# Kernel optimization log

Hardware: AMD Instinct MI355X
Metric: run time of the kernel (lower is better)

Reference implementation:

```python
import jax, jax.numpy as jnp
import numpy as np


def setup_inputs() -> dict:
    key = jax.random.key(0)
    k1, k2 = jax.random.split(key)
    B, S, K, N = 2, 4096, 4096, 4096
    x = jax.random.randint(k1, (B, S, K), -127, 128, dtype=jnp.int32).astype(jnp.int8)
    weight = jax.random.randint(k2, (N, K), -127, 128, dtype=jnp.int32).astype(jnp.int8)
    bias = jnp.zeros((1, N), dtype=jnp.int8)
    a = jnp.float32(0.01)   # alpha = input_scale * weight_scale / output_scale
    b = jnp.float32(1.0)    # beta = bias_scale / output_scale
    return {"x": x, "weight": weight, "bias": bias, "a": a, "b": b}


def reference(x, weight, bias, a, b):
    # i8gemm.linear_a8_w8_b8_o8: int8 GEMM with int32 accumulation, then
    # y_int8 = saturate_cast(round(alpha * acc + beta * bias)).
    x_shape = x.shape
    xf = x.reshape(-1, x_shape[-1])                     # [M, K] int8
    acc = jnp.matmul(xf, weight.T, preferred_element_type=jnp.int32)  # [M, N]
    y = a * acc.astype(jnp.float32) + b * bias.astype(jnp.float32)    # fused epilogue
    yq = jnp.clip(jnp.round(y), -128.0, 127.0).astype(jnp.int8)       # requantize o8
    return yq.reshape(*x_shape[:-1], -1)
```

## Files before the change

### kernel.cpp

```cpp
#include <hip/hip_runtime.h>
#include <stdint.h>

#define M_DIM 8192
#define N_DIM 4096
#define K_DIM 4096

using int4v = __attribute__((ext_vector_type(4))) int;

__global__ __launch_bounds__(256) void pack_kernel(const int4* __restrict__ sx,
                                                   const int4* __restrict__ sw,
                                                   unsigned int* __restrict__ dst,
                                                   int nx, int ntot) {
    int idx = blockIdx.x * blockDim.x + threadIdx.x;
    if (idx >= ntot) return;
    int4 v = (idx < nx) ? sx[idx] : sw[idx - nx];
    dst[idx] = (v.x & 0xff) | ((v.y & 0xff) << 8) | ((v.z & 0xff) << 16) |
               ((v.w & 0xff) << 24);
}

__device__ __forceinline__ void async_copy16(const char* g, char* l) {
    __builtin_amdgcn_global_load_lds(
        (const __attribute__((address_space(1))) char*)g,
        (__attribute__((address_space(3))) char*)l, 16, 0, 0);
}

__global__ __launch_bounds__(256, 2) void gemm_i8_kernel(
    const char* __restrict__ Aq,
    const char* __restrict__ Bq,
    const int* __restrict__ bias,
    const float* __restrict__ a_ptr,
    const float* __restrict__ b_ptr,
    int32_t* __restrict__ out)
{
    __shared__ char As[128 * 64];
    __shared__ char Bs[256 * 64];

    const int tid  = threadIdx.x;
    const int lane = tid & 63;
    const int wave = tid >> 6;
    const int wr   = wave >> 1;
    const int wc   = wave & 1;
    const int m0   = blockIdx.y * 128;
    const int n0   = blockIdx.x * 256;

    const float alpha = *a_ptr;
    const float beta  = *b_ptr;

    int4v acc[4][8] = {};

    const int srow = tid >> 2;
    const int scol = ((tid & 3) ^ ((srow >> 1) & 3)) * 16;

    const char* aG0 = Aq + (size_t)(m0 + srow) * K_DIM + scol;
    const char* aG1 = aG0 + (size_t)64 * K_DIM;
    const char* bG0 = Bq + (size_t)(n0 + srow) * K_DIM + scol;
    const char* bG1 = bG0 + (size_t)64 * K_DIM;
    const char* bG2 = bG0 + (size_t)128 * K_DIM;
    const char* bG3 = bG0 + (size_t)192 * K_DIM;
    char* aL0 = &As[tid * 16];
    char* aL1 = &As[tid * 16 + 4096];
    char* bL0 = &Bs[tid * 16];
    char* bL1 = &Bs[tid * 16 + 4096];
    char* bL2 = &Bs[tid * 16 + 8192];
    char* bL3 = &Bs[tid * 16 + 12288];

    const int fr  = lane & 15;
    const int gw  = lane >> 4;
    const int fko = (gw ^ ((fr >> 1) & 3)) * 16;

    for (int k0 = 0; k0 < K_DIM; k0 += 64) {
        async_copy16(aG0 + k0, aL0);
        async_copy16(aG1 + k0, aL1);
        async_copy16(bG0 + k0, bL0);
        async_copy16(bG1 + k0, bL1);
        async_copy16(bG2 + k0, bL2);
        async_copy16(bG3 + k0, bL3);
        __syncthreads();

        int4v af[4], bf[8];
#pragma unroll
        for (int i = 0; i < 4; ++i)
            af[i] = *(const int4v*)&As[(wr * 64 + i * 16 + fr) * 64 + fko];
#pragma unroll
        for (int j = 0; j < 8; ++j)
            bf[j] = *(const int4v*)&Bs[(wc * 128 + j * 16 + fr) * 64 + fko];

#pragma unroll
        for (int i = 0; i < 4; ++i)
#pragma unroll
            for (int j = 0; j < 8; ++j)
                acc[i][j] = __builtin_amdgcn_mfma_i32_16x16x64_i8(
                    af[i], bf[j], acc[i][j], 0, 0, 0);

        __syncthreads();
    }

    const int orow = (lane >> 4) * 4;
    const int ocol = lane & 15;
#pragma unroll
    for (int j = 0; j < 8; ++j) {
        const int gn = n0 + wc * 128 + j * 16 + ocol;
        const float bb = beta * (float)bias[gn];
#pragma unroll
        for (int i = 0; i < 4; ++i) {
            const int gm = m0 + wr * 64 + i * 16 + orow;
#pragma unroll
            for (int r = 0; r < 4; ++r) {
                float v = alpha * (float)acc[i][j][r] + bb;
                v = rintf(v);
                v = fminf(fmaxf(v, -128.0f), 127.0f);
                out[(size_t)(gm + r) * N_DIM + gn] = (int32_t)v;
            }
        }
    }
}

extern "C" void kernel_launch(void* const* d_in, const int* in_sizes, int n_in,
                              void* d_out, int out_size, void* d_ws, size_t ws_size,
                              hipStream_t stream) {
    const int*   x    = (const int*)d_in[0];
    const int*   w    = (const int*)d_in[1];
    const int*   bias = (const int*)d_in[2];
    const float* a    = (const float*)d_in[3];
    const float* b    = (const float*)d_in[4];
    int32_t*     out  = (int32_t*)d_out;

    char* xq = (char*)d_ws;
    const int nx   = (M_DIM * K_DIM) / 4;
    const int nw   = (N_DIM * K_DIM) / 4;
    const int ntot = nx + nw;
    pack_kernel<<<(ntot + 255) / 256, 256, 0, stream>>>(
        (const int4*)x, (const int4*)w, (unsigned int*)xq, nx, ntot);

    char* wq = xq + (size_t)M_DIM * K_DIM;

    dim3 grid(N_DIM / 256, M_DIM / 128);
    gemm_i8_kernel<<<grid, 256, 0, stream>>>(xq, wq, bias, a, b, out);
}
```

Measured before the change: 403.0 us.

## Rewrite int8 GEMM with 256x256x128 double-buffered ping-pong pipeline and block swizzle

The block tile grows to 256x256 with 512 threads and a K step of 128. A and B shared-memory tiles are now double-buffered, and the async global-to-LDS copies are interleaved with MFMA phases using explicit barriers, waitcnts, sched_barriers and setprio. The grid becomes 1D with a tile swizzle to improve L2 locality. The goal is to hide global load latency and raise arithmetic intensity. The cost is 128KB of LDS and a fragile hand-tuned schedule.

```diff
diff --git a/kernel.cpp b/kernel.cpp
--- a/kernel.cpp
+++ b/kernel.cpp
@@ -24,7 +24,7 @@
         (__attribute__((address_space(3))) char*)l, 16, 0, 0);
 }
 
-__global__ __launch_bounds__(256, 2) void gemm_i8_kernel(
+__global__ __launch_bounds__(512, 2) void gemm_i8_kernel(
     const char* __restrict__ Aq,
     const char* __restrict__ Bq,
     const int* __restrict__ bias,
@@ -32,78 +32,216 @@
     const float* __restrict__ b_ptr,
     int32_t* __restrict__ out)
 {
-    __shared__ char As[128 * 64];
-    __shared__ char Bs[256 * 64];
+    __shared__ char As[2][256 * 128];
+    __shared__ char Bs[2][256 * 128];
 
     const int tid  = threadIdx.x;
     const int lane = tid & 63;
     const int wave = tid >> 6;
-    const int wr   = wave >> 1;
-    const int wc   = wave & 1;
-    const int m0   = blockIdx.y * 128;
-    const int n0   = blockIdx.x * 256;
+    const int wr   = wave >> 2;
+    const int wc   = wave & 3;
+
+    const int bid    = blockIdx.x;
+    const int swzb   = (bid & 7) * 64 + (bid >> 3);
+    const int tile_m = swzb & 31;
+    const int tile_n = swzb >> 5;
+    const int m0 = tile_m * 256;
+    const int n0 = tile_n * 256;
 
     const float alpha = *a_ptr;
     const float beta  = *b_ptr;
 
-    int4v acc[4][8] = {};
-
-    const int srow = tid >> 2;
-    const int scol = ((tid & 3) ^ ((srow >> 1) & 3)) * 16;
-
-    const char* aG0 = Aq + (size_t)(m0 + srow) * K_DIM + scol;
-    const char* aG1 = aG0 + (size_t)64 * K_DIM;
-    const char* bG0 = Bq + (size_t)(n0 + srow) * K_DIM + scol;
-    const char* bG1 = bG0 + (size_t)64 * K_DIM;
-    const char* bG2 = bG0 + (size_t)128 * K_DIM;
-    const char* bG3 = bG0 + (size_t)192 * K_DIM;
-    char* aL0 = &As[tid * 16];
-    char* aL1 = &As[tid * 16 + 4096];
-    char* bL0 = &Bs[tid * 16];
-    char* bL1 = &Bs[tid * 16 + 4096];
-    char* bL2 = &Bs[tid * 16 + 8192];
-    char* bL3 = &Bs[tid * 16 + 12288];
-
-    const int fr  = lane & 15;
-    const int gw  = lane >> 4;
-    const int fko = (gw ^ ((fr >> 1) & 3)) * 16;
-
-    for (int k0 = 0; k0 < K_DIM; k0 += 64) {
-        async_copy16(aG0 + k0, aL0);
-        async_copy16(aG1 + k0, aL1);
-        async_copy16(bG0 + k0, bL0);
-        async_copy16(bG1 + k0, bL1);
-        async_copy16(bG2 + k0, bL2);
-        async_copy16(bG3 + k0, bL3);
-        __syncthreads();
-
-        int4v af[4], bf[8];
-#pragma unroll
-        for (int i = 0; i < 4; ++i)
-            af[i] = *(const int4v*)&As[(wr * 64 + i * 16 + fr) * 64 + fko];
-#pragma unroll
-        for (int j = 0; j < 8; ++j)
-            bf[j] = *(const int4v*)&Bs[(wc * 128 + j * 16 + fr) * 64 + fko];
-
-#pragma unroll
-        for (int i = 0; i < 4; ++i)
-#pragma unroll
-            for (int j = 0; j < 8; ++j)
-                acc[i][j] = __builtin_amdgcn_mfma_i32_16x16x64_i8(
-                    af[i], bf[j], acc[i][j], 0, 0, 0);
-
-        __syncthreads();
+    int4v acc[8][4] = {};
+    int4v rA[8], rB0[4], rB1[4];
+
+    const int fr = lane & 15;
+    const int gw = lane >> 4;
+    const int swz = (fr >> 1) & 7;
+    const int k0off = (gw ^ swz) << 4;
+    const int k1off = ((4 + gw) ^ swz) << 4;
+    const int arow = wr * 128 + fr;
+    const int brow = wc * 64 + fr;
+
+    const int srow = tid >> 3;
+    const int scg  = ((tid & 7) ^ ((tid >> 4) & 7)) << 4;
+    const char* gA0 = Aq + (size_t)(m0 + srow) * K_DIM + scg;
+    const char* gA1 = gA0 + (size_t)64 * K_DIM;
+    const char* gB0 = Bq + (size_t)(n0 + srow) * K_DIM + scg;
+    const char* gB1 = gB0 + (size_t)64 * K_DIM;
+
+#define STAGE_A(buf, h, t)                                                   \
+    do {                                                                     \
+        const size_t off_ = (size_t)(h) * (128 * K_DIM) + (size_t)(t) * 128; \
+        char* l_ = &As[buf][(h)*16384 + (tid << 4)];                         \
+        async_copy16(gA0 + off_, l_);                                        \
+        async_copy16(gA1 + off_, l_ + 8192);                                 \
+    } while (0)
+
+#define STAGE_B(buf, h, t)                                                   \
+    do {                                                                     \
+        const size_t off_ = (size_t)(h) * (128 * K_DIM) + (size_t)(t) * 128; \
+        char* l_ = &Bs[buf][(h)*16384 + (tid << 4)];                         \
+        async_copy16(gB0 + off_, l_);                                        \
+        async_copy16(gB1 + off_, l_ + 8192);                                 \
+    } while (0)
+
+#define DS_A(qm)                                                             \
+    do {                                                                     \
+        _Pragma("unroll") for (int ii = 0; ii < 4; ++ii) {                   \
+            const char* p_ = &As[b][(arow + ((qm)*4 + ii) * 16) * 128];      \
+            rA[ii * 2 + 0] = *(const int4v*)(p_ + k0off);                    \
+            rA[ii * 2 + 1] = *(const int4v*)(p_ + k1off);                    \
+        }                                                                    \
+    } while (0)
+
+#define DS_B(RB, qn)                                                         \
+    do {                                                                     \
+        _Pragma("unroll") for (int jj = 0; jj < 2; ++jj) {                   \
+            const char* p_ = &Bs[b][(brow + ((qn)*2 + jj) * 16) * 128];      \
+            RB[jj * 2 + 0] = *(const int4v*)(p_ + k0off);                    \
+            RB[jj * 2 + 1] = *(const int4v*)(p_ + k1off);                    \
+        }                                                                    \
+    } while (0)
+
+#define MM(qm, qn, RB)                                                       \
+    do {                                                                     \
+        _Pragma("unroll") for (int ii = 0; ii < 4; ++ii)                     \
+        _Pragma("unroll") for (int jj = 0; jj < 2; ++jj)                     \
+        _Pragma("unroll") for (int kk = 0; kk < 2; ++kk)                     \
+            acc[(qm)*4 + ii][(qn)*2 + jj] =                                  \
+                __builtin_amdgcn_mfma_i32_16x16x64_i8(                       \
+                    rA[ii * 2 + kk], RB[jj * 2 + kk],                        \
+                    acc[(qm)*4 + ii][(qn)*2 + jj], 0, 0, 0);                 \
+    } while (0)
+
+#define PH_OPEN                                                              \
+    __builtin_amdgcn_s_barrier();                                            \
+    asm volatile("s_waitcnt lgkmcnt(0)" ::: "memory");                       \
+    __builtin_amdgcn_sched_barrier(0);                                       \
+    __builtin_amdgcn_s_setprio(1)
+
+#define PH_CLOSE                                                             \
+    __builtin_amdgcn_s_setprio(0);                                           \
+    __builtin_amdgcn_s_barrier();                                            \
+    __builtin_amdgcn_sched_barrier(0)
+
+#define PH_CLOSE_VM(n)                                                       \
+    __builtin_amdgcn_s_setprio(0);                                           \
+    asm volatile("s_waitcnt vmcnt(" #n ")" ::: "memory");                    \
+    __builtin_amdgcn_s_barrier();                                            \
+    __builtin_amdgcn_sched_barrier(0)
+
+    STAGE_A(0, 0, 0);
+    STAGE_A(0, 1, 0);
+    STAGE_B(0, 0, 0);
+    STAGE_B(0, 1, 0);
+    STAGE_A(1, 0, 1);
+    asm volatile("s_waitcnt vmcnt(2)" ::: "memory");
+    __builtin_amdgcn_s_barrier();
+    __builtin_amdgcn_sched_barrier(0);
+
+#pragma unroll 1
+    for (int it = 0; it < 15; ++it) {
+        const int t1 = 2 * it + 1;
+        const int t2 = 2 * it + 2;
+        const int t3 = 2 * it + 3;
+        {
+            const int b = 0;
+            DS_A(0); DS_B(rB0, 0);
+            STAGE_A(1, 1, t1);
+            PH_OPEN; MM(0, 0, rB0); PH_CLOSE;
+        }
+        {
+            const int b = 0;
+            DS_B(rB1, 1);
+            STAGE_B(1, 0, t1);
+            STAGE_B(1, 1, t1);
+            PH_OPEN; MM(0, 1, rB1); PH_CLOSE;
+        }
+        {
+            const int b = 0;
+            DS_A(1);
+            PH_OPEN; MM(1, 0, rB0); PH_CLOSE;
+        }
+        {
+            STAGE_A(0, 0, t2);
+            __builtin_amdgcn_s_barrier();
+            __builtin_amdgcn_s_setprio(1);
+            MM(1, 1, rB1);
+            PH_CLOSE_VM(2);
+        }
+        {
+            const int b = 1;
+            DS_A(0); DS_B(rB0, 0);
+            STAGE_A(0, 1, t2);
+            PH_OPEN; MM(0, 0, rB0); PH_CLOSE;
+        }
+        {
+            const int b = 1;
+            DS_B(rB1, 1);
+            STAGE_B(0, 0, t2);
+            STAGE_B(0, 1, t2);
+            PH_OPEN; MM(0, 1, rB1); PH_CLOSE;
+        }
+        {
+            const int b = 1;
+            DS_A(1);
+            PH_OPEN; MM(1, 0, rB0); PH_CLOSE;
+        }
+        {
+            STAGE_A(1, 0, t3);
+            __builtin_amdgcn_s_barrier();
+            __builtin_amdgcn_s_setprio(1);
+            MM(1, 1, rB1);
+            PH_CLOSE_VM(2);
+        }
+    }
+
+    {
+        const int b = 0;
+        {
+            DS_A(0); DS_B(rB0, 0);
+            STAGE_A(1, 1, 31);
+            PH_OPEN; MM(0, 0, rB0); PH_CLOSE;
+        }
+        {
+            DS_B(rB1, 1);
+            STAGE_B(1, 0, 31);
+            STAGE_B(1, 1, 31);
+            PH_OPEN; MM(0, 1, rB1); PH_CLOSE;
+        }
+        {
+            DS_A(1);
+            PH_OPEN; MM(1, 0, rB0); PH_CLOSE;
+        }
+        {
+            __builtin_amdgcn_s_barrier();
+            __builtin_amdgcn_s_setprio(1);
+            MM(1, 1, rB1);
+            PH_CLOSE_VM(0);
+        }
+    }
+    {
+        const int b = 1;
+        DS_A(0); DS_B(rB0, 0); DS_B(rB1, 1);
+        asm volatile("s_waitcnt lgkmcnt(0)" ::: "memory");
+        __builtin_amdgcn_sched_barrier(0);
+        MM(0, 0, rB0); MM(0, 1, rB1);
+        DS_A(1);
+        asm volatile("s_waitcnt lgkmcnt(0)" ::: "memory");
+        __builtin_amdgcn_sched_barrier(0);
+        MM(1, 0, rB0); MM(1, 1, rB1);
     }
 
     const int orow = (lane >> 4) * 4;
     const int ocol = lane & 15;
 #pragma unroll
-    for (int j = 0; j < 8; ++j) {
-        const int gn = n0 + wc * 128 + j * 16 + ocol;
+    for (int j = 0; j < 4; ++j) {
+        const int gn = n0 + wc * 64 + j * 16 + ocol;
         const float bb = beta * (float)bias[gn];
 #pragma unroll
-        for (int i = 0; i < 4; ++i) {
-            const int gm = m0 + wr * 64 + i * 16 + orow;
+        for (int i = 0; i < 8; ++i) {
+            const int gm = m0 + wr * 128 + i * 16 + orow;
 #pragma unroll
             for (int r = 0; r < 4; ++r) {
                 float v = alpha * (float)acc[i][j][r] + bb;
@@ -134,6 +272,6 @@
 
     char* wq = xq + (size_t)M_DIM * K_DIM;
 
-    dim3 grid(N_DIM / 256, M_DIM / 128);
-    gemm_i8_kernel<<<grid, 256, 0, stream>>>(xq, wq, bias, a, b, out);
-}
+    dim3 grid((M_DIM / 256) * (N_DIM / 256));
+    gemm_i8_kernel<<<grid, 512, 0, stream>>>(xq, wq, bias, a, b, out);
+}
```

Result: no change. 405.0 us (+0.5%).

## Use 256x256x128 double-buffered tiles with 8 waves and XCD-aware block mapping

Applied to the files above, without the earlier changes.

Moves the int8 GEMM from a single-buffered 128x256x64 tile with 4 waves to a 256x256 tile with 128-deep K, 8 waves, and two LDS buffers. The next tile's global loads are issued before the current tile is computed, so one barrier per tile replaces two. Blocks are remapped so each XCD works on a contiguous region of M and N to improve L2 reuse, and setprio plus sched_barrier shape the MFMA schedule. The cost is 128KB of LDS per block, which limits occupancy to one block per CU, along with higher register pressure from the 8x4 accumulators.

```diff
diff --git a/kernel.cpp b/kernel.cpp
--- a/kernel.cpp
+++ b/kernel.cpp
@@ -24,7 +24,7 @@
         (__attribute__((address_space(3))) char*)l, 16, 0, 0);
 }
 
-__global__ __launch_bounds__(256, 2) void gemm_i8_kernel(
+__global__ __launch_bounds__(512, 2) void gemm_i8_kernel(
     const char* __restrict__ Aq,
     const char* __restrict__ Bq,
     const int* __restrict__ bias,
@@ -32,78 +32,149 @@
     const float* __restrict__ b_ptr,
     int32_t* __restrict__ out)
 {
-    __shared__ char As[128 * 64];
-    __shared__ char Bs[256 * 64];
+    __shared__ char As0[256 * 128];
+    __shared__ char As1[256 * 128];
+    __shared__ char Bs0[256 * 128];
+    __shared__ char Bs1[256 * 128];
 
     const int tid  = threadIdx.x;
     const int lane = tid & 63;
     const int wave = tid >> 6;
-    const int wr   = wave >> 1;
-    const int wc   = wave & 1;
-    const int m0   = blockIdx.y * 128;
-    const int n0   = blockIdx.x * 256;
+    const int wr   = wave >> 2;
+    const int wc   = wave & 3;
+
+    const int bid = blockIdx.x;
+    const int xcd = bid & 7;
+    const int lin = bid >> 3;
+    const int m0  = ((xcd & 3) * 8 + (lin & 7)) * 256;
+    const int n0  = ((xcd >> 2) * 8 + (lin >> 3)) * 256;
 
     const float alpha = *a_ptr;
     const float beta  = *b_ptr;
 
-    int4v acc[4][8] = {};
-
-    const int srow = tid >> 2;
-    const int scol = ((tid & 3) ^ ((srow >> 1) & 3)) * 16;
-
-    const char* aG0 = Aq + (size_t)(m0 + srow) * K_DIM + scol;
-    const char* aG1 = aG0 + (size_t)64 * K_DIM;
-    const char* bG0 = Bq + (size_t)(n0 + srow) * K_DIM + scol;
-    const char* bG1 = bG0 + (size_t)64 * K_DIM;
-    const char* bG2 = bG0 + (size_t)128 * K_DIM;
-    const char* bG3 = bG0 + (size_t)192 * K_DIM;
-    char* aL0 = &As[tid * 16];
-    char* aL1 = &As[tid * 16 + 4096];
-    char* bL0 = &Bs[tid * 16];
-    char* bL1 = &Bs[tid * 16 + 4096];
-    char* bL2 = &Bs[tid * 16 + 8192];
-    char* bL3 = &Bs[tid * 16 + 12288];
-
-    const int fr  = lane & 15;
-    const int gw  = lane >> 4;
-    const int fko = (gw ^ ((fr >> 1) & 3)) * 16;
-
-    for (int k0 = 0; k0 < K_DIM; k0 += 64) {
-        async_copy16(aG0 + k0, aL0);
-        async_copy16(aG1 + k0, aL1);
-        async_copy16(bG0 + k0, bL0);
-        async_copy16(bG1 + k0, bL1);
-        async_copy16(bG2 + k0, bL2);
-        async_copy16(bG3 + k0, bL3);
-        __syncthreads();
-
-        int4v af[4], bf[8];
-#pragma unroll
-        for (int i = 0; i < 4; ++i)
-            af[i] = *(const int4v*)&As[(wr * 64 + i * 16 + fr) * 64 + fko];
-#pragma unroll
-        for (int j = 0; j < 8; ++j)
-            bf[j] = *(const int4v*)&Bs[(wc * 128 + j * 16 + fr) * 64 + fko];
-
-#pragma unroll
-        for (int i = 0; i < 4; ++i)
-#pragma unroll
-            for (int j = 0; j < 8; ++j)
-                acc[i][j] = __builtin_amdgcn_mfma_i32_16x16x64_i8(
-                    af[i], bf[j], acc[i][j], 0, 0, 0);
-
-        __syncthreads();
-    }
+    int4v acc[8][4] = {};
+
+    const int fr = lane & 15;
+    const int gw = lane >> 4;
+    const int swz = (fr >> 1) & 7;
+    const int k0off = (gw ^ swz) << 4;
+    const int k1off = ((4 + gw) ^ swz) << 4;
+    const int arow = wr * 128 + fr;
+    const int brow = wc * 64 + fr;
+
+    const int srow = tid >> 3;
+    const int scg  = ((tid & 7) ^ ((tid >> 4) & 7)) << 4;
+    const char* gA0 = Aq + (size_t)(m0 + srow) * K_DIM + scg;
+    const char* gA1 = gA0 + (size_t)64 * K_DIM;
+    const char* gB0 = Bq + (size_t)(n0 + srow) * K_DIM + scg;
+    const char* gB1 = gB0 + (size_t)64 * K_DIM;
+
+#define STAGE_A(AS, h, t)                                                    \
+    {                                                                        \
+        const size_t off_ = (size_t)(h) * (128 * K_DIM) + (size_t)(t) * 128; \
+        char* l_ = &AS[(h)*16384 + (tid << 4)];                              \
+        async_copy16(gA0 + off_, l_);                                        \
+        async_copy16(gA1 + off_, l_ + 8192);                                 \
+    }
+
+#define STAGE_B(BS, h, t)                                                    \
+    {                                                                        \
+        const size_t off_ = (size_t)(h) * (128 * K_DIM) + (size_t)(t) * 128; \
+        char* l_ = &BS[(h)*16384 + (tid << 4)];                              \
+        async_copy16(gB0 + off_, l_);                                        \
+        async_copy16(gB1 + off_, l_ + 8192);                                 \
+    }
+
+#define STAGE_TILE(AS, BS, t)                                                \
+    {                                                                        \
+        STAGE_A(AS, 0, t);                                                   \
+        STAGE_A(AS, 1, t);                                                   \
+        STAGE_B(BS, 0, t);                                                   \
+        STAGE_B(BS, 1, t);                                                   \
+    }
+
+#define DS_A2(AS, qm)                                                        \
+    {                                                                        \
+        _Pragma("unroll") for (int ii = 0; ii < 4; ++ii) {                   \
+            const char* pa_ = &AS[(arow + ((qm)*4 + ii) * 16) * 128];        \
+            af[ii * 2 + 0] = *(const int4v*)(pa_ + k0off);                   \
+            af[ii * 2 + 1] = *(const int4v*)(pa_ + k1off);                   \
+        }                                                                    \
+    }
+
+#define DS_B2(BS, R, qn)                                                     \
+    {                                                                        \
+        _Pragma("unroll") for (int jj = 0; jj < 2; ++jj) {                   \
+            const char* pb_ = &BS[(brow + ((qn)*2 + jj) * 16) * 128];        \
+            R[jj * 2 + 0] = *(const int4v*)(pb_ + k0off);                    \
+            R[jj * 2 + 1] = *(const int4v*)(pb_ + k1off);                    \
+        }                                                                    \
+    }
+
+#define MM2(qm, qn, RB)                                                      \
+    {                                                                        \
+        _Pragma("unroll") for (int ii = 0; ii < 4; ++ii)                     \
+        _Pragma("unroll") for (int jj = 0; jj < 2; ++jj)                     \
+        _Pragma("unroll") for (int kk = 0; kk < 2; ++kk)                     \
+            acc[(qm)*4 + ii][(qn)*2 + jj] =                                  \
+                __builtin_amdgcn_mfma_i32_16x16x64_i8(                       \
+                    af[ii * 2 + kk], RB[jj * 2 + kk],                        \
+                    acc[(qm)*4 + ii][(qn)*2 + jj], 0, 0, 0);                 \
+    }
+
+#define COMPUTE_TILE(AS, BS)                                                 \
+    {                                                                        \
+        int4v af[8], bf0[4], bf1[4];                                         \
+        DS_A2(AS, 0);                                                        \
+        DS_B2(BS, bf0, 0);                                                   \
+        DS_B2(BS, bf1, 1);                                                   \
+        __builtin_amdgcn_s_setprio(1);                                       \
+        MM2(0, 0, bf0);                                                      \
+        MM2(0, 1, bf1);                                                      \
+        DS_A2(AS, 1);                                                        \
+        MM2(1, 0, bf0);                                                      \
+        MM2(1, 1, bf1);                                                      \
+        __builtin_amdgcn_s_setprio(0);                                       \
+    }
+
+#define TILE_END                                                             \
+    {                                                                        \
+        asm volatile("s_waitcnt vmcnt(0)" ::: "memory");                     \
+        __builtin_amdgcn_s_barrier();                                        \
+        __builtin_amdgcn_sched_barrier(0);                                   \
+    }
+
+    STAGE_TILE(As0, Bs0, 0);
+    TILE_END;
+
+#pragma unroll 1
+    for (int it = 0; it < 15; ++it) {
+        const int t1 = 2 * it + 1;
+        const int t2 = 2 * it + 2;
+        STAGE_TILE(As1, Bs1, t1);
+        __builtin_amdgcn_sched_barrier(0);
+        COMPUTE_TILE(As0, Bs0);
+        TILE_END;
+        STAGE_TILE(As0, Bs0, t2);
+        __builtin_amdgcn_sched_barrier(0);
+        COMPUTE_TILE(As1, Bs1);
+        TILE_END;
+    }
+    STAGE_TILE(As1, Bs1, 31);
+    __builtin_amdgcn_sched_barrier(0);
+    COMPUTE_TILE(As0, Bs0);
+    TILE_END;
+    COMPUTE_TILE(As1, Bs1);
 
     const int orow = (lane >> 4) * 4;
     const int ocol = lane & 15;
 #pragma unroll
-    for (int j = 0; j < 8; ++j) {
-        const int gn = n0 + wc * 128 + j * 16 + ocol;
+    for (int j = 0; j < 4; ++j) {
+        const int gn = n0 + wc * 64 + j * 16 + ocol;
         const float bb = beta * (float)bias[gn];
 #pragma unroll
-        for (int i = 0; i < 4; ++i) {
-            const int gm = m0 + wr * 64 + i * 16 + orow;
+        for (int i = 0; i < 8; ++i) {
+            const int gm = m0 + wr * 128 + i * 16 + orow;
 #pragma unroll
             for (int r = 0; r < 4; ++r) {
                 float v = alpha * (float)acc[i][j][r] + bb;
@@ -134,6 +205,6 @@
 
     char* wq = xq + (size_t)M_DIM * K_DIM;
 
-    dim3 grid(N_DIM / 256, M_DIM / 128);
-    gemm_i8_kernel<<<grid, 256, 0, stream>>>(xq, wq, bias, a, b, out);
-}
+    dim3 grid((M_DIM / 256) * (N_DIM / 256));
+    gemm_i8_kernel<<<grid, 512, 0, stream>>>(xq, wq, bias, a, b, out);
+}
```

Result: faster. 394.9 us (-2.0%).

## Double-buffer LDS tiles with 512-thread blocks, 256x128 tiles and XCD-aware mapping

Applied to the files above, without the earlier changes.

Switches the GEMM to 256x128 output tiles computed by 8 waves, each holding a 64x64 accumulator. LDS is double-buffered so the async global-to-LDS load of the next K slice is issued before the MFMAs on the current slice, with one barrier per step instead of two. It also remaps the 1D block index so blocks sharing the same A/B tiles land on the same XCD, and raises wave priority around the MFMA bursts. This trades fewer accumulators per wave and more LDS per block for better overlap of loads with compute and better L2 reuse.

```diff
diff --git a/kernel.cpp b/kernel.cpp
--- a/kernel.cpp
+++ b/kernel.cpp
@@ -24,7 +24,7 @@
         (__attribute__((address_space(3))) char*)l, 16, 0, 0);
 }
 
-__global__ __launch_bounds__(256, 2) void gemm_i8_kernel(
+__global__ __launch_bounds__(512, 4) void gemm_i8_kernel(
     const char* __restrict__ Aq,
     const char* __restrict__ Bq,
     const int* __restrict__ bias,
@@ -32,74 +32,97 @@
     const float* __restrict__ b_ptr,
     int32_t* __restrict__ out)
 {
-    __shared__ char As[128 * 64];
-    __shared__ char Bs[256 * 64];
+    __shared__ char As0[256 * 64];
+    __shared__ char As1[256 * 64];
+    __shared__ char Bs0[128 * 64];
+    __shared__ char Bs1[128 * 64];
 
     const int tid  = threadIdx.x;
     const int lane = tid & 63;
     const int wave = tid >> 6;
     const int wr   = wave >> 1;
     const int wc   = wave & 1;
-    const int m0   = blockIdx.y * 128;
-    const int n0   = blockIdx.x * 256;
+
+    const int bid = blockIdx.x;
+    const int xcd = bid & 7;
+    const int lin = bid >> 3;
+    const int mt  = (xcd & 3) * 8 + (lin & 7);
+    const int nt  = (xcd >> 2) * 16 + (lin >> 3);
+    const int m0  = mt * 256;
+    const int n0  = nt * 128;
 
     const float alpha = *a_ptr;
     const float beta  = *b_ptr;
 
-    int4v acc[4][8] = {};
+    int4v acc[4][4] = {};
+
+    const int fr   = lane & 15;
+    const int gw   = lane >> 4;
+    const int koff = ((gw ^ ((fr >> 1) & 3)) << 4);
+    const int aoff = (wr * 64 + fr) * 64 + koff;
+    const int boff = (wc * 64 + fr) * 64 + koff;
 
     const int srow = tid >> 2;
-    const int scol = ((tid & 3) ^ ((srow >> 1) & 3)) * 16;
+    const int scg  = ((tid & 3) ^ ((tid >> 3) & 3)) << 4;
+    const char* gA0 = Aq + (size_t)(m0 + srow) * K_DIM + scg;
+    const char* gA1 = gA0 + (size_t)128 * K_DIM;
+    const char* gB0 = Bq + (size_t)(n0 + srow) * K_DIM + scg;
 
-    const char* aG0 = Aq + (size_t)(m0 + srow) * K_DIM + scol;
-    const char* aG1 = aG0 + (size_t)64 * K_DIM;
-    const char* bG0 = Bq + (size_t)(n0 + srow) * K_DIM + scol;
-    const char* bG1 = bG0 + (size_t)64 * K_DIM;
-    const char* bG2 = bG0 + (size_t)128 * K_DIM;
-    const char* bG3 = bG0 + (size_t)192 * K_DIM;
-    char* aL0 = &As[tid * 16];
-    char* aL1 = &As[tid * 16 + 4096];
-    char* bL0 = &Bs[tid * 16];
-    char* bL1 = &Bs[tid * 16 + 4096];
-    char* bL2 = &Bs[tid * 16 + 8192];
-    char* bL3 = &Bs[tid * 16 + 12288];
+#define STAGE(AS, BS, t)                                                     \
+    {                                                                        \
+        const size_t off_ = (size_t)(t) * 64;                                \
+        async_copy16(gA0 + off_, &AS[tid * 16]);                             \
+        async_copy16(gA1 + off_, &AS[8192 + tid * 16]);                      \
+        async_copy16(gB0 + off_, &BS[tid * 16]);                             \
+    }
 
-    const int fr  = lane & 15;
-    const int gw  = lane >> 4;
-    const int fko = (gw ^ ((fr >> 1) & 3)) * 16;
+#define COMPUTE(AS, BS)                                                      \
+    {                                                                        \
+        int4v af[4], bf[4];                                                  \
+        _Pragma("unroll") for (int i = 0; i < 4; ++i)                        \
+            af[i] = *(const int4v*)&AS[aoff + i * 1024];                     \
+        _Pragma("unroll") for (int j = 0; j < 4; ++j)                        \
+            bf[j] = *(const int4v*)&BS[boff + j * 1024];                     \
+        __builtin_amdgcn_s_setprio(1);                                       \
+        _Pragma("unroll") for (int i = 0; i < 4; ++i)                        \
+        _Pragma("unroll") for (int j = 0; j < 4; ++j)                        \
+            acc[i][j] = __builtin_amdgcn_mfma_i32_16x16x64_i8(               \
+                af[i], bf[j], acc[i][j], 0, 0, 0);                           \
+        __builtin_amdgcn_s_setprio(0);                                       \
+    }
 
-    for (int k0 = 0; k0 < K_DIM; k0 += 64) {
-        async_copy16(aG0 + k0, aL0);
-        async_copy16(aG1 + k0, aL1);
-        async_copy16(bG0 + k0, bL0);
-        async_copy16(bG1 + k0, bL1);
-        async_copy16(bG2 + k0, bL2);
-        async_copy16(bG3 + k0, bL3);
-        __syncthreads();
+#define STEP_END                                                             \
+    {                                                                        \
+        asm volatile("s_waitcnt vmcnt(0)" ::: "memory");                     \
+        __builtin_amdgcn_s_barrier();                                        \
+        __builtin_amdgcn_sched_barrier(0);                                   \
+    }
 
-        int4v af[4], bf[8];
-#pragma unroll
-        for (int i = 0; i < 4; ++i)
-            af[i] = *(const int4v*)&As[(wr * 64 + i * 16 + fr) * 64 + fko];
-#pragma unroll
-        for (int j = 0; j < 8; ++j)
-            bf[j] = *(const int4v*)&Bs[(wc * 128 + j * 16 + fr) * 64 + fko];
+    STAGE(As0, Bs0, 0);
+    STEP_END;
 
-#pragma unroll
-        for (int i = 0; i < 4; ++i)
-#pragma unroll
-            for (int j = 0; j < 8; ++j)
-                acc[i][j] = __builtin_amdgcn_mfma_i32_16x16x64_i8(
-                    af[i], bf[j], acc[i][j], 0, 0, 0);
-
-        __syncthreads();
+#pragma unroll 1
+    for (int it = 0; it < 31; ++it) {
+        STAGE(As1, Bs1, 2 * it + 1);
+        __builtin_amdgcn_sched_barrier(0);
+        COMPUTE(As0, Bs0);
+        STEP_END;
+        STAGE(As0, Bs0, 2 * it + 2);
+        __builtin_amdgcn_sched_barrier(0);
+        COMPUTE(As1, Bs1);
+        STEP_END;
     }
+    STAGE(As1, Bs1, 63);
+    __builtin_amdgcn_sched_barrier(0);
+    COMPUTE(As0, Bs0);
+    STEP_END;
+    COMPUTE(As1, Bs1);
 
     const int orow = (lane >> 4) * 4;
     const int ocol = lane & 15;
 #pragma unroll
-    for (int j = 0; j < 8; ++j) {
-        const int gn = n0 + wc * 128 + j * 16 + ocol;
+    for (int j = 0; j < 4; ++j) {
+        const int gn = n0 + wc * 64 + j * 16 + ocol;
         const float bb = beta * (float)bias[gn];
 #pragma unroll
         for (int i = 0; i < 4; ++i) {
@@ -134,6 +157,6 @@
 
     char* wq = xq + (size_t)M_DIM * K_DIM;
 
-    dim3 grid(N_DIM / 256, M_DIM / 128);
-    gemm_i8_kernel<<<grid, 256, 0, stream>>>(xq, wq, bias, a, b, out);
+    dim3 grid((M_DIM / 256) * (N_DIM / 128));
+    gemm_i8_kernel<<<grid, 512, 0, stream>>>(xq, wq, bias, a, b, out);
 }
```

After: 408.1 us. Within noise of the previous version (+1.3%).
